# Kernel tuning notes

Measured on AMD Instinct MI355X. Metric: run time of the kernel, lower is better.

The kernel has to match this reference:

```python
import jax, jax.numpy as jnp
import numpy as np

D_MODEL = 1024
N_HEAD = 16
D_HEAD = D_MODEL // N_HEAD
D_FF = 4096
EPS = 1e-5


def _layernorm(x, gamma, beta):
    mu = jnp.mean(x, axis=-1, keepdims=True)
    var = jnp.mean(jnp.square(x - mu), axis=-1, keepdims=True)
    return (x - mu) * jax.lax.rsqrt(var + EPS) * gamma + beta


def setup_inputs() -> dict:
    key = jax.random.key(0)
    ks = jax.random.split(key, 16)
    s = 1.0 / np.sqrt(D_MODEL)
    sf = 1.0 / np.sqrt(D_FF)
    return {
        "src": jax.random.normal(ks[0], (8, 1024, D_MODEL), dtype=jnp.float32),
        "Wq": jax.random.uniform(ks[1], (D_MODEL, D_MODEL), jnp.float32, -s, s),
        "bq": jnp.zeros((D_MODEL,), jnp.float32),
        "Wk": jax.random.uniform(ks[2], (D_MODEL, D_MODEL), jnp.float32, -s, s),
        "bk": jnp.zeros((D_MODEL,), jnp.float32),
        "Wv": jax.random.uniform(ks[3], (D_MODEL, D_MODEL), jnp.float32, -s, s),
        "bv": jnp.zeros((D_MODEL,), jnp.float32),
        "Wo": jax.random.uniform(ks[4], (D_MODEL, D_MODEL), jnp.float32, -s, s),
        "bo": jnp.zeros((D_MODEL,), jnp.float32),
        "W1": jax.random.uniform(ks[5], (D_MODEL, D_FF), jnp.float32, -s, s),
        "b1": jnp.zeros((D_FF,), jnp.float32),
        "W2": jax.random.uniform(ks[6], (D_FF, D_MODEL), jnp.float32, -sf, sf),
        "b2": jnp.zeros((D_MODEL,), jnp.float32),
        "g1": jnp.ones((D_MODEL,), jnp.float32),
        "beta1": jnp.zeros((D_MODEL,), jnp.float32),
        "g2": jnp.ones((D_MODEL,), jnp.float32),
        "beta2": jnp.zeros((D_MODEL,), jnp.float32),
    }


def reference(src, Wq, bq, Wk, bk, Wv, bv, Wo, bo, W1, b1, W2, b2, g1, beta1, g2, beta2):
    B, S, _ = src.shape
    x = _layernorm(src, g1, beta1)
    # QKV projections -> [B, H, S, Dh]
    def split_heads(t):
        return t.reshape(B, S, N_HEAD, D_HEAD).transpose(0, 2, 1, 3)
    q = split_heads(x @ Wq + bq)
    k = split_heads(x @ Wk + bk)
    v = split_heads(x @ Wv + bv)
    # SymbolicAttention (canonical graph): softmax(q k^T / sqrt(d_head)) v
    scores = jnp.einsum('bhqd,bhkd->bhqk', q, k) / np.sqrt(D_HEAD).astype(np.float32)
    attn = jax.nn.softmax(scores, axis=-1)
    ctx = jnp.einsum('bhqk,bhkd->bhqd', attn, v)
    ctx = ctx.transpose(0, 2, 1, 3).reshape(B, S, D_MODEL)
    src = src + (ctx @ Wo + bo)  # dropout is identity in eval
    y = _layernorm(src, g2, beta2)
    ffn = jax.nn.relu(y @ W1 + b1) @ W2 + b2
    return src + ffn
```

## Files before the change

### kernel.cpp

```cpp
#include <hip/hip_runtime.h>
#include <stdint.h>

#define D_MODEL 1024
#define N_HEAD  16
#define D_HEAD  64
#define D_FF    4096
#define SEQ     1024
#define BATCH   8
#define M_TOK   (BATCH*SEQ)

typedef __attribute__((ext_vector_type(8))) short bf16x8;
typedef __attribute__((ext_vector_type(4))) float f32x4;

__device__ __forceinline__ float bf2f(unsigned short u) {
    union { unsigned int u; float f; } x; x.u = ((unsigned int)u) << 16; return x.f;
}
__device__ __forceinline__ unsigned short f2bf(float f) {
    union { float f; unsigned int u; } x; x.f = f;
    unsigned int r = x.u + 0x7fffu + ((x.u >> 16) & 1u);
    return (unsigned short)(r >> 16);
}

typedef const __attribute__((address_space(1))) unsigned int* gas_t;
typedef __attribute__((address_space(3))) unsigned int* las_t;
__device__ __forceinline__ void gl_lds16(const unsigned short* g, unsigned short* l) {
    __builtin_amdgcn_global_load_lds((gas_t)g, (las_t)l, 16, 0, 0);
}

#define DSR(dst, addr, IMM) \
    asm volatile("ds_read_b128 %0, %1 offset:" #IMM : "=v"(dst) : "v"(addr))

__global__ __launch_bounds__(256) void transpose_cvt(
        const float* __restrict__ src, unsigned short* __restrict__ dst,
        int R, int C)
{
    __shared__ float t[32][33];
    const int tx = threadIdx.x & 31, ty = threadIdx.x >> 5;
    const int c0 = blockIdx.x * 32, r0 = blockIdx.y * 32;
    #pragma unroll
    for (int i = 0; i < 32; i += 8)
        t[ty + i][tx] = src[(size_t)(r0 + ty + i) * C + c0 + tx];
    __syncthreads();
    #pragma unroll
    for (int i = 0; i < 32; i += 8)
        dst[(size_t)(c0 + ty + i) * R + r0 + tx] = f2bf(t[tx][ty + i]);
}

__global__ __launch_bounds__(256) void ln_kernel(
        const float* __restrict__ x, const float* __restrict__ g,
        const float* __restrict__ be, unsigned short* __restrict__ out)
{
    const int row = blockIdx.x, tid = threadIdx.x;
    const f32x4 v = *(const f32x4*)(x + (size_t)row * D_MODEL + tid * 4);
    float s  = v[0] + v[1] + v[2] + v[3];
    float ss = v[0]*v[0] + v[1]*v[1] + v[2]*v[2] + v[3]*v[3];
    #pragma unroll
    for (int o = 1; o < 64; o <<= 1) { s += __shfl_xor(s, o); ss += __shfl_xor(ss, o); }
    __shared__ float sa[4], sb[4];
    const int wv = tid >> 6;
    if ((tid & 63) == 0) { sa[wv] = s; sb[wv] = ss; }
    __syncthreads();
    s  = sa[0] + sa[1] + sa[2] + sa[3];
    ss = sb[0] + sb[1] + sb[2] + sb[3];
    const float mu   = s * (1.0f / D_MODEL);
    const float rstd = rsqrtf(ss * (1.0f / D_MODEL) - mu * mu + 1e-5f);
    const f32x4 gv = *(const f32x4*)(g  + tid * 4);
    const f32x4 bv = *(const f32x4*)(be + tid * 4);
    unsigned short w[4];
    #pragma unroll
    for (int j = 0; j < 4; j++) w[j] = f2bf((v[j] - mu) * rstd * gv[j] + bv[j]);
    *(uint2*)(out + (size_t)row * D_MODEL + tid * 4) = *(uint2*)w;
}

template<int MODE>
__global__ __launch_bounds__(512, 2) void gemm256(
        const unsigned short* __restrict__ A,
        const unsigned short* __restrict__ BT,
        const float* __restrict__ b1_,
        const float* __restrict__ b2_,
        const float* __restrict__ b3_,
        void* __restrict__ Cout,
        int M, int N, int K)
{
    (void)M;
    __shared__ unsigned short As[32768];
    __shared__ unsigned short Bs[32768];

    const int tid  = threadIdx.x;
    const int wave = tid >> 6, lane = tid & 63;
    const int quad = lane >> 4, l16 = lane & 15;
    const int wm = wave >> 2, wn = wave & 3;

    const int nbx = gridDim.x;
    const int bid = blockIdx.x + nbx * blockIdx.y;
    const int chunk = (nbx * gridDim.y) >> 3;
    const int lg = (bid & 7) * chunk + (bid >> 3);
    const int m0 = (lg / nbx) * 256;
    const int n0 = (lg % nbx) * 256;
    const int NT = K >> 6;

    const int st_row = tid >> 3;
    const int st_g   = (tid & 7) ^ (st_row & 7);
    const unsigned short* gA = A  + (size_t)(m0 + st_row) * K + st_g * 8;
    const unsigned short* gB = BT + (size_t)(n0 + st_row) * K + st_g * 8;
    unsigned short* lA = As + wave * 512;
    unsigned short* lB = Bs + wave * 512;

    const unsigned asBase = (unsigned)(size_t)(las_t)(void*)As;
    const unsigned bsBase = (unsigned)(size_t)(las_t)(void*)Bs;
    const unsigned aOff = (unsigned)((wm * 64 + l16) * 128);
    const unsigned bOff = (unsigned)((wn * 32 + l16) * 128);
    const unsigned s0b  = (unsigned)((quad ^ (l16 & 7)) * 16);
    const unsigned s1b  = s0b ^ 64;

    f32x4 acc[8][4] = {};

#define STAGE_A(T, H, D) \
    do { gl_lds16(gA + (size_t)((H)*128   )*K + (size_t)(T)*64, lA + (D)*16384 + (H)*8192); \
         gl_lds16(gA + (size_t)((H)*128+64)*K + (size_t)(T)*64, lA + (D)*16384 + (H)*8192 + 4096); } while(0)
#define STAGE_B(T, H, D) \
    do { gl_lds16(gB + (size_t)((H)*128   )*K + (size_t)(T)*64, lB + (D)*16384 + (H)*8192); \
         gl_lds16(gB + (size_t)((H)*128+64)*K + (size_t)(T)*64, lB + (D)*16384 + (H)*8192 + 4096); } while(0)

    STAGE_A(0, 0, 0); STAGE_B(0, 0, 0); STAGE_B(0, 1, 0); STAGE_A(0, 1, 0);
    STAGE_A(1, 0, 1); STAGE_B(1, 0, 1); STAGE_B(1, 1, 1);
    asm volatile("s_waitcnt vmcnt(6)" ::: "memory");
    __builtin_amdgcn_s_barrier();
    asm volatile("" ::: "memory");

    for (int t = 0; t < NT; ++t) {
        const int db = t & 1;
        const unsigned dbo = (unsigned)(db * 32768);
        const unsigned aR0 = asBase + dbo + aOff + s0b;
        const unsigned aR1 = asBase + dbo + aOff + s1b;
        const unsigned bR0 = bsBase + dbo + bOff + s0b;
        const unsigned bR1 = bsBase + dbo + bOff + s1b;
        bf16x8 a0[4], a1[4], bA0[2], bA1[2], bB0[2], bB1[2];

        DSR(a0[0], aR0, 0);    DSR(a0[1], aR0, 2048);
        DSR(a0[2], aR0, 4096); DSR(a0[3], aR0, 6144);
        DSR(a1[0], aR1, 0);    DSR(a1[1], aR1, 2048);
        DSR(a1[2], aR1, 4096); DSR(a1[3], aR1, 6144);
        DSR(bA0[0], bR0, 0);   DSR(bA0[1], bR0, 2048);
        DSR(bA1[0], bR1, 0);   DSR(bA1[1], bR1, 2048);
        if (t + 1 < NT) STAGE_A(t + 1, 1, db ^ 1);
        asm volatile("" ::: "memory");
        __builtin_amdgcn_s_barrier();
        asm volatile("s_waitcnt lgkmcnt(0)" ::: "memory");
        __builtin_amdgcn_sched_barrier(0);
        __builtin_amdgcn_s_setprio(1);
        #pragma unroll
        for (int mi = 0; mi < 4; ++mi)
            #pragma unroll
            for (int ni = 0; ni < 2; ++ni)
                acc[mi][ni] = __builtin_amdgcn_mfma_f32_16x16x32_bf16(
                        bA0[ni], a0[mi], acc[mi][ni], 0, 0, 0);
        #pragma unroll
        for (int mi = 0; mi < 4; ++mi)
            #pragma unroll
            for (int ni = 0; ni < 2; ++ni)
                acc[mi][ni] = __builtin_amdgcn_mfma_f32_16x16x32_bf16(
                        bA1[ni], a1[mi], acc[mi][ni], 0, 0, 0);
        __builtin_amdgcn_s_setprio(0);
        asm volatile("" ::: "memory");
        __builtin_amdgcn_s_barrier();

        DSR(bB0[0], bR0, 16384);   DSR(bB0[1], bR0, 18432);
        DSR(bB1[0], bR1, 16384);   DSR(bB1[1], bR1, 18432);
        if (t + 2 < NT) STAGE_A(t + 2, 0, db);
        asm volatile("" ::: "memory");
        __builtin_amdgcn_s_barrier();
        asm volatile("s_waitcnt lgkmcnt(0)" ::: "memory");
        __builtin_amdgcn_sched_barrier(0);
        __builtin_amdgcn_s_setprio(1);
        #pragma unroll
        for (int mi = 0; mi < 4; ++mi)
            #pragma unroll
            for (int ni = 0; ni < 2; ++ni)
                acc[mi][2 + ni] = __builtin_amdgcn_mfma_f32_16x16x32_bf16(
                        bB0[ni], a0[mi], acc[mi][2 + ni], 0, 0, 0);
        #pragma unroll
        for (int mi = 0; mi < 4; ++mi)
            #pragma unroll
            for (int ni = 0; ni < 2; ++ni)
                acc[mi][2 + ni] = __builtin_amdgcn_mfma_f32_16x16x32_bf16(
                        bB1[ni], a1[mi], acc[mi][2 + ni], 0, 0, 0);
        __builtin_amdgcn_s_setprio(0);
        asm volatile("" ::: "memory");
        __builtin_amdgcn_s_barrier();

        DSR(a0[0], aR0, 16384); DSR(a0[1], aR0, 18432);
        DSR(a0[2], aR0, 20480); DSR(a0[3], aR0, 22528);
        DSR(a1[0], aR1, 16384); DSR(a1[1], aR1, 18432);
        DSR(a1[2], aR1, 20480); DSR(a1[3], aR1, 22528);
        if (t + 2 < NT) STAGE_B(t + 2, 0, db);
        asm volatile("" ::: "memory");
        __builtin_amdgcn_s_barrier();
        asm volatile("s_waitcnt lgkmcnt(0)" ::: "memory");
        __builtin_amdgcn_sched_barrier(0);
        __builtin_amdgcn_s_setprio(1);
        #pragma unroll
        for (int mi = 0; mi < 4; ++mi)
            #pragma unroll
            for (int ni = 0; ni < 2; ++ni)
                acc[4 + mi][ni] = __builtin_amdgcn_mfma_f32_16x16x32_bf16(
                        bA0[ni], a0[mi], acc[4 + mi][ni], 0, 0, 0);
        #pragma unroll
        for (int mi = 0; mi < 4; ++mi)
            #pragma unroll
            for (int ni = 0; ni < 2; ++ni)
                acc[4 + mi][ni] = __builtin_amdgcn_mfma_f32_16x16x32_bf16(
                        bA1[ni], a1[mi], acc[4 + mi][ni], 0, 0, 0);
        __builtin_amdgcn_s_setprio(0);
        asm volatile("" ::: "memory");
        __builtin_amdgcn_s_barrier();

        if (t + 2 < NT) {
            STAGE_B(t + 2, 1, db);
            asm volatile("s_waitcnt vmcnt(6)" ::: "memory");
        } else {
            asm volatile("s_waitcnt vmcnt(0)" ::: "memory");
        }
        __builtin_amdgcn_s_barrier();
        __builtin_amdgcn_s_setprio(1);
        #pragma unroll
        for (int mi = 0; mi < 4; ++mi)
            #pragma unroll
            for (int ni = 0; ni < 2; ++ni)
                acc[4 + mi][2 + ni] = __builtin_amdgcn_mfma_f32_16x16x32_bf16(
                        bB0[ni], a0[mi], acc[4 + mi][2 + ni], 0, 0, 0);
        #pragma unroll
        for (int mi = 0; mi < 4; ++mi)
            #pragma unroll
            for (int ni = 0; ni < 2; ++ni)
                acc[4 + mi][2 + ni] = __builtin_amdgcn_mfma_f32_16x16x32_bf16(
                        bB1[ni], a1[mi], acc[4 + mi][2 + ni], 0, 0, 0);
        __builtin_amdgcn_s_setprio(0);
        asm volatile("" ::: "memory");
        __builtin_amdgcn_s_barrier();
    }
#undef STAGE_A
#undef STAGE_B

    if (MODE == 1) {
        unsigned short* dst = (unsigned short*)Cout;
        #pragma unroll
        for (int f = 0; f < 8; ++f) {
            const int row = m0 + (f >> 2) * 128 + wm * 64 + (f & 3) * 16 + l16;
            #pragma unroll
            for (int g = 0; g < 4; ++g) {
                const int col = n0 + (g >> 1) * 128 + wn * 32 + (g & 1) * 16 + quad * 4;
                const f32x4 bs4 = *(const f32x4*)(b1_ + col);
                unsigned short w[4];
                #pragma unroll
                for (int r = 0; r < 4; ++r)
                    w[r] = f2bf(fmaxf(acc[f][g][r] + bs4[r], 0.0f));
                *(uint2*)(dst + (size_t)row * N + col) = *(uint2*)w;
            }
        }
    } else {
        const int rt = n0 >> 10;
        if (rt < 2) {
            unsigned short* dst = (unsigned short*)Cout + (size_t)rt * M_TOK * 1024;
            const float sc = (rt == 0) ? 0.125f : 1.0f;
            const float* bs = (rt == 0) ? b1_ : b2_;
            const int nb = n0 & 1023;
            #pragma unroll
            for (int f = 0; f < 8; ++f) {
                const int row = m0 + (f >> 2) * 128 + wm * 64 + (f & 3) * 16 + l16;
                #pragma unroll
                for (int g = 0; g < 4; ++g) {
                    const int col = nb + (g >> 1) * 128 + wn * 32 + (g & 1) * 16 + quad * 4;
                    const f32x4 bs4 = *(const f32x4*)(bs + col);
                    unsigned short w[4];
                    #pragma unroll
                    for (int r = 0; r < 4; ++r)
                        w[r] = f2bf((acc[f][g][r] + bs4[r]) * sc);
                    *(uint2*)(dst + (size_t)row * 1024 + col) = *(uint2*)w;
                }
            }
        } else {
            unsigned short* vdst = (unsigned short*)Cout + (size_t)2 * M_TOK * 1024;
            const int nb = n0 - 2048;
            #pragma unroll
            for (int f = 0; f < 8; ++f) {
                const int row = m0 + (f >> 2) * 128 + wm * 64 + (f & 3) * 16 + l16;
                const int bb = row >> 10, s = row & 1023;
                #pragma unroll
                for (int g = 0; g < 4; ++g) {
                    const int cc = nb + (g >> 1) * 128 + wn * 32 + (g & 1) * 16 + quad * 4;
                    #pragma unroll
                    for (int r = 0; r < 4; ++r)
                        vdst[((size_t)(bb * 1024 + cc + r)) * 1024 + s]
                            = f2bf(acc[f][g][r] + b3_[cc + r]);
                }
            }
        }
    }
}

template<int MODE>
__global__ __launch_bounds__(256) void gemm_bf16_tn(
        const unsigned short* __restrict__ A,
        const unsigned short* __restrict__ BT,
        const float* __restrict__ bias,
        const float* __restrict__ bias2,
        const float* __restrict__ bias3,
        const float* __restrict__ resid,
        void* __restrict__ Cout,
        int M, int N, int K)
{
    (void)bias2; (void)bias3;
    __shared__ unsigned short As[128 * 64];
    __shared__ unsigned short Bs[128 * 64];

    const int tid  = threadIdx.x;
    const int wave = tid >> 6, lane = tid & 63;
    const int quad = lane >> 4, l16 = lane & 15;

    int m0, n0;
    if (MODE == 2) {
        const int G = gridDim.x;
        const int f = blockIdx.x + G * blockIdx.y;
        m0 = ((f & 7) + 8 * ((f >> 3) / G)) * 128;
        n0 = ((f >> 3) % G) * 128;
    } else {
        m0 = blockIdx.y * 128;
        n0 = blockIdx.x * 128;
    }
    const int wm = (wave >> 1) * 64, wn = (wave & 1) * 64;

    const int st_row = wave * 8 + ((tid >> 3) & 7);
    const int st_g   = (tid & 7) ^ ((tid >> 3) & 7);
    const unsigned short* gA = A  + (size_t)(m0 + st_row) * K + st_g * 8;
    const unsigned short* gB = BT + (size_t)(n0 + st_row) * K + st_g * 8;
    unsigned short* lA = As + wave * 512;
    unsigned short* lB = Bs + wave * 512;
    const int rx = l16 & 7;

    f32x4 acc[4][4] = {};

    for (int k0 = 0; k0 < K; k0 += 64) {
        __syncthreads();
        #pragma unroll
        for (int j = 0; j < 4; j++) {
            gl_lds16(gA + (size_t)j * 32 * K + k0, lA + j * 2048);
            gl_lds16(gB + (size_t)j * 32 * K + k0, lB + j * 2048);
        }
        __syncthreads();

        #pragma unroll
        for (int h = 0; h < 2; h++) {
            bf16x8 af[4], bfr[4];
            #pragma unroll
            for (int mi = 0; mi < 4; mi++)
                af[mi] = *(const bf16x8*)(As + (wm + mi * 16 + l16) * 64
                                          + ((h * 4 + quad) ^ rx) * 8);
            #pragma unroll
            for (int ni = 0; ni < 4; ni++)
                bfr[ni] = *(const bf16x8*)(Bs + (wn + ni * 16 + l16) * 64
                                           + ((h * 4 + quad) ^ rx) * 8);
            #pragma unroll
            for (int mi = 0; mi < 4; mi++)
                #pragma unroll
                for (int ni = 0; ni < 4; ni++)
                    acc[mi][ni] = __builtin_amdgcn_mfma_f32_16x16x32_bf16(
                              bfr[ni], af[mi], acc[mi][ni], 0, 0, 0);
        }
    }

    #pragma unroll
    for (int mi = 0; mi < 4; mi++) {
        const int row = m0 + wm + mi * 16 + l16;
        #pragma unroll
        for (int ni = 0; ni < 4; ni++) {
            const int col = n0 + wn + ni * 16 + quad * 4;
            const f32x4 bs4 = *(const f32x4*)(bias + col);
            const f32x4 rv = *(const f32x4*)(resid + (size_t)row * N + col);
            f32x4 o;
            #pragma unroll
            for (int r = 0; r < 4; r++)
                o[r] = acc[mi][ni][r] + bs4[r] + rv[r];
            *(f32x4*)((float*)Cout + (size_t)row * N + col) = o;
        }
    }
}

#define ASTR 72
__global__ __launch_bounds__(256) void attn_mfma(
        const unsigned short* __restrict__ Q,
        const unsigned short* __restrict__ K,
        const unsigned short* __restrict__ VT,
        unsigned short* __restrict__ CTX)
{
    __shared__ unsigned short Ks[64 * ASTR];
    __shared__ unsigned short Vs[64 * ASTR];
    __shared__ unsigned short Ps[128 * ASTR];

    const int tid  = threadIdx.x;
    const int wave = tid >> 6, lane = tid & 63;
    const int quad = lane >> 4, l16 = lane & 15;
    const int bh = blockIdx.y;
    const int q0 = blockIdx.x * 128;
    const size_t baseQ = (size_t)(bh >> 4) * SEQ * D_MODEL + (size_t)(bh & 15) * D_HEAD;
    const size_t baseV = (size_t)bh * D_HEAD * SEQ;
    const int strip = wave * 32;

    bf16x8 qf[2][2];
    #pragma unroll
    for (int mt = 0; mt < 2; mt++)
        #pragma unroll
        for (int h = 0; h < 2; h++)
            qf[mt][h] = *(const bf16x8*)(Q + baseQ
                        + (size_t)(q0 + strip + mt * 16 + l16) * D_MODEL
                        + h * 32 + quad * 8);

    f32x4 of[2][4] = {};
    float l_p[2][4] = {};

    for (int c = 0; c < SEQ / 64; c++) {
        const int k0 = c * 64;
        __syncthreads();
        #pragma unroll
        for (int u = tid; u < 512; u += 256) {
            const int r = u >> 3, g = (u & 7) * 8;
            *(uint4*)(Ks + r * ASTR + g) =
                *(const uint4*)(K + baseQ + (size_t)(k0 + r) * D_MODEL + g);
            *(uint4*)(Vs + r * ASTR + g) =
                *(const uint4*)(VT + baseV + (size_t)r * SEQ + k0 + g);
        }
        __syncthreads();

        bf16x8 kf[4][2];
        #pragma unroll
        for (int kt = 0; kt < 4; kt++)
            #pragma unroll
            for (int h = 0; h < 2; h++)
                kf[kt][h] = *(const bf16x8*)(Ks + (kt * 16 + l16) * ASTR + h * 32 + quad * 8);

        #pragma unroll
        for (int mt = 0; mt < 2; mt++) {
            f32x4 s[4] = {};
            #pragma unroll
            for (int h = 0; h < 2; h++)
                #pragma unroll
                for (int kt = 0; kt < 4; kt++)
                    s[kt] = __builtin_amdgcn_mfma_f32_16x16x32_bf16(
                            qf[mt][h], kf[kt][h], s[kt], 0, 0, 0);
            #pragma unroll
            for (int kt = 0; kt < 4; kt++)
                #pragma unroll
                for (int r = 0; r < 4; r++) {
                    const float p = __expf(s[kt][r]);
                    l_p[mt][r] += p;
                    Ps[(strip + mt * 16 + quad * 4 + r) * ASTR + kt * 16 + l16] = f2bf(p);
                }
        }

        bf16x8 pf[2][2];
        #pragma unroll
        for (int mt = 0; mt < 2; mt++)
            #pragma unroll
            for (int h = 0; h < 2; h++)
                pf[mt][h] = *(const bf16x8*)(Ps + (strip + mt * 16 + l16) * ASTR
                                             + h * 32 + quad * 8);
        #pragma unroll
        for (int nt = 0; nt < 4; nt++) {
            bf16x8 vf[2];
            #pragma unroll
            for (int h = 0; h < 2; h++)
                vf[h] = *(const bf16x8*)(Vs + (nt * 16 + l16) * ASTR + h * 32 + quad * 8);
            #pragma unroll
            for (int mt = 0; mt < 2; mt++)
                #pragma unroll
                for (int h = 0; h < 2; h++)
                    of[mt][nt] = __builtin_amdgcn_mfma_f32_16x16x32_bf16(
                            pf[mt][h], vf[h], of[mt][nt], 0, 0, 0);
        }
    }

    #pragma unroll
    for (int mt = 0; mt < 2; mt++) {
        float inv[4];
        #pragma unroll
        for (int r = 0; r < 4; r++) {
            float l = l_p[mt][r];
            #pragma unroll
            for (int o = 1; o < 16; o <<= 1) l += __shfl_xor(l, o);
            inv[r] = 1.0f / l;
        }
        #pragma unroll
        for (int nt = 0; nt < 4; nt++)
            #pragma unroll
            for (int r = 0; r < 4; r++)
                CTX[baseQ + (size_t)(q0 + strip + mt * 16 + quad * 4 + r) * D_MODEL
                    + nt * 16 + l16] = f2bf(of[mt][nt][r] * inv[r]);
    }
}

extern "C" void kernel_launch(void* const* d_in, const int* in_sizes, int n_in,
                              void* d_out, int out_size, void* d_ws, size_t ws_size,
                              hipStream_t stream)
{
    (void)in_sizes; (void)n_in; (void)out_size; (void)ws_size;
    const float* src = (const float*)d_in[0];
    const float* Wq  = (const float*)d_in[1];
    const float* bq  = (const float*)d_in[2];
    const float* Wk  = (const float*)d_in[3];
    const float* bk  = (const float*)d_in[4];
    const float* Wv  = (const float*)d_in[5];
    const float* bv  = (const float*)d_in[6];
    const float* Wo  = (const float*)d_in[7];
    const float* bo  = (const float*)d_in[8];
    const float* W1  = (const float*)d_in[9];
    const float* b1  = (const float*)d_in[10];
    const float* W2  = (const float*)d_in[11];
    const float* b2  = (const float*)d_in[12];
    const float* g1  = (const float*)d_in[13];
    const float* be1 = (const float*)d_in[14];
    const float* g2  = (const float*)d_in[15];
    const float* be2 = (const float*)d_in[16];
    float* out = (float*)d_out;

    unsigned short* wqkvT = (unsigned short*)d_ws;
    unsigned short* woT = wqkvT + (size_t)3 * 1024 * 1024;
    unsigned short* w1T = woT + 1024 * 1024;
    unsigned short* w2T = w1T + (size_t)4096 * 1024;
    unsigned short* xn  = w2T + (size_t)1024 * 4096;
    unsigned short* q   = xn  + (size_t)M_TOK * D_MODEL;
    unsigned short* k   = q   + (size_t)M_TOK * D_MODEL;
    unsigned short* vT  = k   + (size_t)M_TOK * D_MODEL;
    unsigned short* ctx = vT  + (size_t)M_TOK * D_MODEL;
    unsigned short* hid = ctx + (size_t)M_TOK * D_MODEL;

    const dim3 blk(256);
    const dim3 blk512(512);

    transpose_cvt<<<dim3(32, 32),  blk, 0, stream>>>(Wq, wqkvT,                 1024, 1024);
    transpose_cvt<<<dim3(32, 32),  blk, 0, stream>>>(Wk, wqkvT + 1024 * 1024,   1024, 1024);
    transpose_cvt<<<dim3(32, 32),  blk, 0, stream>>>(Wv, wqkvT + 2 * 1024 * 1024, 1024, 1024);
    transpose_cvt<<<dim3(32, 32),  blk, 0, stream>>>(Wo, woT, 1024, 1024);
    transpose_cvt<<<dim3(128, 32), blk, 0, stream>>>(W1, w1T, 1024, 4096);
    transpose_cvt<<<dim3(32, 128), blk, 0, stream>>>(W2, w2T, 4096, 1024);

    ln_kernel<<<M_TOK, blk, 0, stream>>>(src, g1, be1, xn);

    gemm256<3><<<dim3(12, 32), blk512, 0, stream>>>(
        xn, wqkvT, bq, bk, bv, q, M_TOK, 3072, D_MODEL);

    attn_mfma<<<dim3(SEQ / 128, BATCH * N_HEAD), blk, 0, stream>>>(q, k, vT, ctx);

    gemm_bf16_tn<2><<<dim3(8, 64), blk, 0, stream>>>(
        ctx, woT, bo, nullptr, nullptr, src, out, M_TOK, D_MODEL, D_MODEL);

    ln_kernel<<<M_TOK, blk, 0, stream>>>(out, g2, be2, xn);

    gemm256<1><<<dim3(16, 32), blk512, 0, stream>>>(
        xn, w1T, b1, nullptr, nullptr, hid, M_TOK, D_FF, D_MODEL);

    gemm_bf16_tn<2><<<dim3(8, 64), blk, 0, stream>>>(
        hid, w2T, b2, nullptr, nullptr, out, out, M_TOK, D_MODEL, D_FF);
}
```

Before: 497.4 us.

## Replace N=1024 GEMMs with double-buffered 256x128 tile pipelined kernel

Replaces the simple 128x128 single-buffered GEMM used for the output projection and FFN down-projection with a 512-thread kernel computing 256x128 tiles. It double-buffers A and B in LDS, prefetches the next K-tiles while MFMAs run, splits the work into two half-tile phases with explicit waitcnt/barrier scheduling and priority boosts, and uses a grouped block-index remap for L2 locality. The goal is to hide global load latency and improve operand reuse on the two N=1024 GEMMs. In exchange it uses much more LDS (96KB) and relies on hand-tuned vmcnt counts, which makes correctness fragile.

```diff
diff --git a/kernel.cpp b/kernel.cpp
--- a/kernel.cpp
+++ b/kernel.cpp
@@ -299,91 +299,147 @@
     }
 }
 
-template<int MODE>
-__global__ __launch_bounds__(256) void gemm_bf16_tn(
+__global__ __launch_bounds__(512, 2) void gemm_n128(
         const unsigned short* __restrict__ A,
         const unsigned short* __restrict__ BT,
         const float* __restrict__ bias,
-        const float* __restrict__ bias2,
-        const float* __restrict__ bias3,
         const float* __restrict__ resid,
-        void* __restrict__ Cout,
-        int M, int N, int K)
+        float* __restrict__ Cout,
+        int N, int K)
 {
-    (void)bias2; (void)bias3;
-    __shared__ unsigned short As[128 * 64];
-    __shared__ unsigned short Bs[128 * 64];
+    __shared__ unsigned short As[32768];
+    __shared__ unsigned short Bs[16384];
 
     const int tid  = threadIdx.x;
     const int wave = tid >> 6, lane = tid & 63;
     const int quad = lane >> 4, l16 = lane & 15;
-
-    int m0, n0;
-    if (MODE == 2) {
-        const int G = gridDim.x;
-        const int f = blockIdx.x + G * blockIdx.y;
-        m0 = ((f & 7) + 8 * ((f >> 3) / G)) * 128;
-        n0 = ((f >> 3) % G) * 128;
-    } else {
-        m0 = blockIdx.y * 128;
-        n0 = blockIdx.x * 128;
-    }
-    const int wm = (wave >> 1) * 64, wn = (wave & 1) * 64;
-
-    const int st_row = wave * 8 + ((tid >> 3) & 7);
-    const int st_g   = (tid & 7) ^ ((tid >> 3) & 7);
+    const int wm = wave >> 1, wn = wave & 1;
+
+    const int nbx = gridDim.x;
+    const int bid = blockIdx.x + nbx * blockIdx.y;
+    const int chunk = (nbx * gridDim.y) >> 3;
+    const int lg = (bid & 7) * chunk + (bid >> 3);
+    const int m0 = (lg / nbx) * 256;
+    const int n0 = (lg % nbx) * 128;
+    const int NT = K >> 6;
+
+    const int st_row = tid >> 3;
+    const int st_g   = (tid & 7) ^ (st_row & 7);
     const unsigned short* gA = A  + (size_t)(m0 + st_row) * K + st_g * 8;
     const unsigned short* gB = BT + (size_t)(n0 + st_row) * K + st_g * 8;
     unsigned short* lA = As + wave * 512;
     unsigned short* lB = Bs + wave * 512;
-    const int rx = l16 & 7;
+
+    const unsigned asBase = (unsigned)(size_t)(las_t)(void*)As;
+    const unsigned bsBase = (unsigned)(size_t)(las_t)(void*)Bs;
+    const unsigned aOff = (unsigned)((wm * 32 + l16) * 128);
+    const unsigned bOff = (unsigned)((wn * 64 + l16) * 128);
+    const unsigned s0b  = (unsigned)((quad ^ (l16 & 7)) * 16);
+    const unsigned s1b  = s0b ^ 64;
 
     f32x4 acc[4][4] = {};
 
-    for (int k0 = 0; k0 < K; k0 += 64) {
-        __syncthreads();
-        #pragma unroll
-        for (int j = 0; j < 4; j++) {
-            gl_lds16(gA + (size_t)j * 32 * K + k0, lA + j * 2048);
-            gl_lds16(gB + (size_t)j * 32 * K + k0, lB + j * 2048);
-        }
-        __syncthreads();
-
-        #pragma unroll
-        for (int h = 0; h < 2; h++) {
-            bf16x8 af[4], bfr[4];
-            #pragma unroll
-            for (int mi = 0; mi < 4; mi++)
-                af[mi] = *(const bf16x8*)(As + (wm + mi * 16 + l16) * 64
-                                          + ((h * 4 + quad) ^ rx) * 8);
-            #pragma unroll
-            for (int ni = 0; ni < 4; ni++)
-                bfr[ni] = *(const bf16x8*)(Bs + (wn + ni * 16 + l16) * 64
-                                           + ((h * 4 + quad) ^ rx) * 8);
-            #pragma unroll
-            for (int mi = 0; mi < 4; mi++)
+#define STG_A(T, H, D) \
+    do { gl_lds16(gA + (size_t)((H)*128   )*K + (size_t)(T)*64, lA + (D)*16384 + (H)*8192); \
+         gl_lds16(gA + (size_t)((H)*128+64)*K + (size_t)(T)*64, lA + (D)*16384 + (H)*8192 + 4096); } while(0)
+#define STG_B(T, D) \
+    do { gl_lds16(gB + (size_t)(T)*64,                 lB + (D)*8192); \
+         gl_lds16(gB + (size_t)64*K + (size_t)(T)*64,  lB + (D)*8192 + 4096); } while(0)
+
+    STG_A(0, 0, 0); STG_B(0, 0); STG_A(0, 1, 0);
+    STG_A(1, 0, 1); STG_B(1, 1);
+    asm volatile("s_waitcnt vmcnt(6)" ::: "memory");
+    __builtin_amdgcn_s_barrier();
+    asm volatile("" ::: "memory");
+
+    for (int t = 0; t < NT; ++t) {
+        const int db = t & 1;
+        const unsigned aR0 = asBase + (unsigned)(db << 15) + aOff + s0b;
+        const unsigned aR1 = asBase + (unsigned)(db << 15) + aOff + s1b;
+        const unsigned bR0 = bsBase + (unsigned)(db << 14) + bOff + s0b;
+        const unsigned bR1 = bsBase + (unsigned)(db << 14) + bOff + s1b;
+        bf16x8 a0[2][2], a1[2][2], bf[4][2];
+
+        DSR(a0[0][0], aR0, 0);    DSR(a0[1][0], aR0, 2048);
+        DSR(a0[0][1], aR1, 0);    DSR(a0[1][1], aR1, 2048);
+        DSR(bf[0][0], bR0, 0);    DSR(bf[1][0], bR0, 2048);
+        DSR(bf[2][0], bR0, 4096); DSR(bf[3][0], bR0, 6144);
+        DSR(bf[0][1], bR1, 0);    DSR(bf[1][1], bR1, 2048);
+        DSR(bf[2][1], bR1, 4096); DSR(bf[3][1], bR1, 6144);
+        if (t + 1 < NT) STG_A(t + 1, 1, db ^ 1);
+        asm volatile("" ::: "memory");
+        __builtin_amdgcn_s_barrier();
+        asm volatile("s_waitcnt lgkmcnt(0)" ::: "memory");
+        __builtin_amdgcn_sched_barrier(0);
+        __builtin_amdgcn_s_setprio(1);
+        #pragma unroll
+        for (int mi = 0; mi < 2; ++mi)
+            #pragma unroll
+            for (int ni = 0; ni < 4; ++ni)
+                acc[mi][ni] = __builtin_amdgcn_mfma_f32_16x16x32_bf16(
+                        bf[ni][0], a0[mi][0], acc[mi][ni], 0, 0, 0);
+        #pragma unroll
+        for (int mi = 0; mi < 2; ++mi)
+            #pragma unroll
+            for (int ni = 0; ni < 4; ++ni)
+                acc[mi][ni] = __builtin_amdgcn_mfma_f32_16x16x32_bf16(
+                        bf[ni][1], a0[mi][1], acc[mi][ni], 0, 0, 0);
+        __builtin_amdgcn_s_setprio(0);
+        if (t + 1 < NT) asm volatile("s_waitcnt vmcnt(6)" ::: "memory");
+        else            asm volatile("s_waitcnt vmcnt(0)" ::: "memory");
+        __builtin_amdgcn_s_barrier();
+        asm volatile("" ::: "memory");
+
+        DSR(a1[0][0], aR0, 16384); DSR(a1[1][0], aR0, 18432);
+        DSR(a1[0][1], aR1, 16384); DSR(a1[1][1], aR1, 18432);
+        if (t + 2 < NT) { STG_A(t + 2, 0, db); STG_B(t + 2, db); }
+        asm volatile("" ::: "memory");
+        __builtin_amdgcn_s_barrier();
+        asm volatile("s_waitcnt lgkmcnt(0)" ::: "memory");
+        __builtin_amdgcn_sched_barrier(0);
+        __builtin_amdgcn_s_setprio(1);
+        #pragma unroll
+        for (int mi = 0; mi < 2; ++mi)
+            #pragma unroll
+            for (int ni = 0; ni < 4; ++ni)
+                acc[2 + mi][ni] = __builtin_amdgcn_mfma_f32_16x16x32_bf16(
+                        bf[ni][0], a1[mi][0], acc[2 + mi][ni], 0, 0, 0);
+        #pragma unroll
+        for (int mi = 0; mi < 2; ++mi)
+            #pragma unroll
+            for (int ni = 0; ni < 4; ++ni)
+                acc[2 + mi][ni] = __builtin_amdgcn_mfma_f32_16x16x32_bf16(
+                        bf[ni][1], a1[mi][1], acc[2 + mi][ni], 0, 0, 0);
+        __builtin_amdgcn_s_setprio(0);
+        if (t + 2 < NT) {
+            asm volatile("s_waitcnt vmcnt(6)" ::: "memory");
+            __builtin_amdgcn_s_barrier();
+        } else if (t + 1 < NT) {
+            asm volatile("s_waitcnt vmcnt(2)" ::: "memory");
+            __builtin_amdgcn_s_barrier();
+        }
+        asm volatile("" ::: "memory");
+    }
+#undef STG_A
+#undef STG_B
+
+    #pragma unroll
+    for (int qm = 0; qm < 2; ++qm)
+        #pragma unroll
+        for (int mi = 0; mi < 2; ++mi) {
+            const int row = m0 + qm * 128 + wm * 32 + mi * 16 + l16;
+            #pragma unroll
+            for (int ni = 0; ni < 4; ++ni) {
+                const int col = n0 + wn * 64 + ni * 16 + quad * 4;
+                const f32x4 bs4 = *(const f32x4*)(bias + col);
+                const f32x4 rv  = *(const f32x4*)(resid + (size_t)row * N + col);
+                f32x4 o;
                 #pragma unroll
-                for (int ni = 0; ni < 4; ni++)
-                    acc[mi][ni] = __builtin_amdgcn_mfma_f32_16x16x32_bf16(
-                              bfr[ni], af[mi], acc[mi][ni], 0, 0, 0);
-        }
-    }
-
-    #pragma unroll
-    for (int mi = 0; mi < 4; mi++) {
-        const int row = m0 + wm + mi * 16 + l16;
-        #pragma unroll
-        for (int ni = 0; ni < 4; ni++) {
-            const int col = n0 + wn + ni * 16 + quad * 4;
-            const f32x4 bs4 = *(const f32x4*)(bias + col);
-            const f32x4 rv = *(const f32x4*)(resid + (size_t)row * N + col);
-            f32x4 o;
-            #pragma unroll
-            for (int r = 0; r < 4; r++)
-                o[r] = acc[mi][ni][r] + bs4[r] + rv[r];
-            *(f32x4*)((float*)Cout + (size_t)row * N + col) = o;
-        }
-    }
+                for (int r = 0; r < 4; ++r)
+                    o[r] = acc[qm * 2 + mi][ni][r] + bs4[r] + rv[r];
+                *(f32x4*)(Cout + (size_t)row * N + col) = o;
+            }
+        }
 }
 
 #define ASTR 72
@@ -550,14 +606,14 @@
 
     attn_mfma<<<dim3(SEQ / 128, BATCH * N_HEAD), blk, 0, stream>>>(q, k, vT, ctx);
 
-    gemm_bf16_tn<2><<<dim3(8, 64), blk, 0, stream>>>(
-        ctx, woT, bo, nullptr, nullptr, src, out, M_TOK, D_MODEL, D_MODEL);
+    gemm_n128<<<dim3(8, 32), blk512, 0, stream>>>(
+        ctx, woT, bo, src, out, D_MODEL, D_MODEL);
 
     ln_kernel<<<M_TOK, blk, 0, stream>>>(out, g2, be2, xn);
 
     gemm256<1><<<dim3(16, 32), blk512, 0, stream>>>(
         xn, w1T, b1, nullptr, nullptr, hid, M_TOK, D_FF, D_MODEL);
 
-    gemm_bf16_tn<2><<<dim3(8, 64), blk, 0, stream>>>(
-        hid, w2T, b2, nullptr, nullptr, out, out, M_TOK, D_MODEL, D_FF);
-}
+    gemm_n128<<<dim3(8, 32), blk512, 0, stream>>>(
+        hid, w2T, b2, out, out, D_MODEL, D_FF);
+}
```

Measured after the change: 501.3 us. Within noise of the previous version (+0.8%).
